# Performance work log

Measured on AMD Instinct MI355X. Metric: run time of the kernel, lower is better.

Reference implementation:

```python
import jax, jax.numpy as jnp
import numpy as np

TEMP = 0.1
EPS = 1e-12


def setup_inputs() -> dict:
    key = jax.random.key(0)
    k0, k1 = jax.random.split(key)
    instances_view0 = jax.random.normal(k0, (128, 32, 512), dtype=jnp.float32)
    instances_view1 = jax.random.normal(k1, (128, 32, 512), dtype=jnp.float32)
    return {"instances_view0": instances_view0, "instances_view1": instances_view1}


def reference(instances_view0, instances_view1):
    B, I, D = instances_view0.shape
    n_per_view = B * I  # n_instances_per_view
    f0 = instances_view0.reshape(n_per_view, D)
    f1 = instances_view1.reshape(n_per_view, D)
    inst = jnp.concatenate((f0, f1), axis=0)  # [N, D], N = 2*B*I
    # L2 normalize rows (torch F.normalize with eps clamp)
    norm = jnp.maximum(jnp.linalg.norm(inst, axis=1, keepdims=True), EPS)
    z = inst / norm
    sim_exp = jnp.exp(z @ z.T / TEMP)  # [N, N]
    denom = sim_exp.sum(axis=1) - jnp.diagonal(sim_exp)  # exclude self-similarity
    # positives: pairs offset by n_per_view in both directions
    idx = jnp.arange(n_per_view)
    upper = sim_exp[idx, idx + n_per_view]   # diagonal(offset=+n)
    lower = sim_exp[idx + n_per_view, idx]   # diagonal(offset=-n)
    nom = jnp.concatenate((upper, lower), axis=0)  # [N]
    loss = -jnp.log(nom / denom)
    return loss.mean()  # reduction='batchmean'
```

## Files before the change

kernel.cpp:

```cpp
#include <hip/hip_runtime.h>
#include <hip/hip_bf16.h>
#include <cstdint>

#define NROWS 8192
#define NPER  4096
#define DIM   512
#define TEMP_INV 10.0f
#define FP8_SCALE 16.0f
#define DOT_UNSCALE (1.0f / 256.0f)
#define NB    64
#define NBLK  2080
#define PAIR_OFF 32

typedef float f32x4 __attribute__((ext_vector_type(4)));

__global__ __launch_bounds__(256) void k_normalize(const float* __restrict__ v0,
                                                   const float* __restrict__ v1,
                                                   unsigned char* __restrict__ z,
                                                   float* __restrict__ rowsum,
                                                   float* __restrict__ out) {
  if (blockIdx.x < 32) rowsum[blockIdx.x * 256 + threadIdx.x] = 0.f;
  if (blockIdx.x == 0 && threadIdx.x == 0) out[0] = 0.f;
  const int wid  = (blockIdx.x * 256 + threadIdx.x) >> 6;
  const int lane = threadIdx.x & 63;
  if (wid >= NROWS) return;
  const float* src = (wid < NPER) ? (v0 + (size_t)wid * DIM)
                                  : (v1 + (size_t)(wid - NPER) * DIM);
  float4 a = *(const float4*)(src + lane * 8);
  float4 b = *(const float4*)(src + lane * 8 + 4);
  float ss = a.x*a.x + a.y*a.y + a.z*a.z + a.w*a.w
           + b.x*b.x + b.y*b.y + b.z*b.z + b.w*b.w;
  #pragma unroll
  for (int m = 1; m < 64; m <<= 1) ss += __shfl_xor(ss, m);
  float inv = FP8_SCALE / fmaxf(sqrtf(ss), 1e-12f);
  int w0 = __builtin_amdgcn_cvt_pk_fp8_f32(a.x * inv, a.y * inv, 0, false);
  w0     = __builtin_amdgcn_cvt_pk_fp8_f32(a.z * inv, a.w * inv, w0, true);
  int w1 = __builtin_amdgcn_cvt_pk_fp8_f32(b.x * inv, b.y * inv, 0, false);
  w1     = __builtin_amdgcn_cvt_pk_fp8_f32(b.z * inv, b.w * inv, w1, true);
  uint2 p; p.x = (unsigned)w0; p.y = (unsigned)w1;
  *(uint2*)(z + (size_t)wid * DIM + lane * 8) = p;
}

__global__ __launch_bounds__(256, 3) void k_gemm_sym(const unsigned char* __restrict__ z,
                                                     float* __restrict__ rowsum,
                                                     float* __restrict__ s) {
  __shared__ __align__(16) unsigned char As[128 * 128];
  __shared__ __align__(16) unsigned char Bs[128 * 128];

  const int tid  = threadIdx.x;
  const int lane = tid & 63;
  const int w    = tid >> 6;
  const int wr   = w >> 1;
  const int wc   = w & 1;

  const int orig = blockIdx.x;
  const int t = (orig & 7) * (NBLK / 8) + (orig >> 3);

  int a = 0;
  while (a < 7 && 484 * (a + 1) - 32 * (a + 1) * a <= t) ++a;
  int l = t - (484 * a - 32 * a * (a - 1));
  int ri, rj, sj;
  if (l < 36) {
    sj = a;
    ri = 0;
    while (l >= 8 - ri) { l -= 8 - ri; ++ri; }
    rj = ri + l;
  } else {
    l -= 36;
    sj = a + 1 + (l >> 6);
    const int ll = l & 63;
    ri = ll >> 3; rj = ll & 7;
  }
  const int bi = a * 8 + ri;
  const int bj = sj * 8 + rj;
  const int brow = bi * 128;
  const int bcol = bj * 128;
  const bool diag = (bi == bj);
  const bool pair = (bj - bi == PAIR_OFF);

  f32x4 acc[4][4];
  const f32x4 zero = {0.f, 0.f, 0.f, 0.f};
  #pragma unroll
  for (int m = 0; m < 4; ++m)
    #pragma unroll
    for (int n = 0; n < 4; ++n) acc[m][n] = zero;

  const int srow = (lane >> 3);
  const int skof = 16 * ((lane & 7) ^ srow);
  auto stage = [&](int k0) {
    #pragma unroll
    for (int i = 0; i < 4; ++i) {
      const int c = w * 4 + i;
      const int row_in = c * 8 + srow;
      const unsigned char* ga = z + (size_t)(brow + row_in) * DIM + k0 + skof;
      const unsigned char* gb = z + (size_t)(bcol + row_in) * DIM + k0 + skof;
      __builtin_amdgcn_global_load_lds(
          (const __attribute__((address_space(1))) void*)ga,
          (__attribute__((address_space(3))) void*)(&As[c * 1024]), 16, 0, 0);
      __builtin_amdgcn_global_load_lds(
          (const __attribute__((address_space(1))) void*)gb,
          (__attribute__((address_space(3))) void*)(&Bs[c * 1024]), 16, 0, 0);
    }
  };

  const int r0 = lane & 15;
  const int g  = lane >> 4;
  int colk[4];
  #pragma unroll
  for (int kk = 0; kk < 4; ++kk)
    colk[kk] = (((kk * 2 + (g >> 1)) ^ (r0 & 7)) << 4) + ((g & 1) << 3);

  for (int kt = 0; kt < 4; ++kt) {
    stage(kt * 128);
    asm volatile("s_waitcnt vmcnt(0)" ::: "memory");
    __builtin_amdgcn_s_barrier();

    const char* Ab = (const char*)&As[0] + (size_t)(wr * 64 + r0) * 128;
    const char* Bb = (const char*)&Bs[0] + (size_t)(wc * 64 + r0) * 128;
    #pragma unroll
    for (int kk = 0; kk < 4; ++kk) {
      const int cb = colk[kk];
      long bfrag[4];
      #pragma unroll
      for (int n = 0; n < 4; ++n)
        bfrag[n] = *(const long*)(Bb + n * (16 * 128) + cb);
      #pragma unroll
      for (int m = 0; m < 4; ++m) {
        long afrag = *(const long*)(Ab + m * (16 * 128) + cb);
        #pragma unroll
        for (int n = 0; n < 4; ++n)
          acc[m][n] = __builtin_amdgcn_mfma_f32_16x16x32_fp8_fp8(
              afrag, bfrag[n], acc[m][n], 0, 0, 0);
      }
    }
    asm volatile("s_waitcnt lgkmcnt(0)" ::: "memory");
    __builtin_amdgcn_sched_barrier(0);
    __builtin_amdgcn_s_barrier();
  }

  float (*racc)[128] = (float (*)[128])As;
  float (*cacc)[128] = ((float (*)[128])As) + 2;

  float cs[4] = {0.f, 0.f, 0.f, 0.f};
  const int grow0 = brow + wr * 64;
  const int gcol0 = bcol + wc * 64;
  const float expc = TEMP_INV * DOT_UNSCALE;
  #pragma unroll
  for (int m = 0; m < 4; ++m) {
    #pragma unroll
    for (int j = 0; j < 4; ++j) {
      const int grow = grow0 + m * 16 + g * 4 + j;
      float v = 0.f;
      #pragma unroll
      for (int n = 0; n < 4; ++n) {
        const int gcol = gcol0 + n * 16 + r0;
        const float rawacc = acc[m][n][j];
        const float e = __expf(rawacc * expc);
        if (grow != gcol) { v += e; cs[n] += e; }
        if (pair && (grow + NPER == gcol)) {
          const float raw = rawacc * DOT_UNSCALE;
          s[grow] = raw;
          s[gcol] = raw;
        }
      }
      v += __shfl_xor(v, 1);
      v += __shfl_xor(v, 2);
      v += __shfl_xor(v, 4);
      v += __shfl_xor(v, 8);
      if (r0 == 0) racc[wc][wr * 64 + m * 16 + g * 4 + j] = v;
    }
  }
  #pragma unroll
  for (int n = 0; n < 4; ++n) {
    float v = cs[n];
    v += __shfl_xor(v, 16);
    v += __shfl_xor(v, 32);
    if (lane < 16) cacc[wr][wc * 64 + n * 16 + lane] = v;
  }
  __syncthreads();
  if (tid < 128) {
    atomicAdd(&rowsum[brow + tid], racc[0][tid] + racc[1][tid]);
  } else if (!diag) {
    const int i = tid - 128;
    atomicAdd(&rowsum[bcol + i], cacc[0][i] + cacc[1][i]);
  }
}

__global__ __launch_bounds__(256) void k_loss(const float* __restrict__ rowsum,
                                              const float* __restrict__ s,
                                              float* __restrict__ out) {
  __shared__ float red[4];
  const int i = blockIdx.x * 256 + threadIdx.x;
  float v = logf(rowsum[i]) - s[i] * TEMP_INV;
  #pragma unroll
  for (int m = 1; m < 64; m <<= 1) v += __shfl_xor(v, m);
  const int w = threadIdx.x >> 6;
  if ((threadIdx.x & 63) == 0) red[w] = v;
  __syncthreads();
  if (threadIdx.x == 0)
    atomicAdd(out, (red[0] + red[1] + red[2] + red[3]) * (1.0f / (float)NROWS));
}

extern "C" void kernel_launch(void* const* d_in, const int* in_sizes, int n_in,
                              void* d_out, int out_size, void* d_ws, size_t ws_size,
                              hipStream_t stream) {
  const float* v0 = (const float*)d_in[0];
  const float* v1 = (const float*)d_in[1];
  float* out = (float*)d_out;

  unsigned char* z = (unsigned char*)d_ws;
  float* rowsum = (float*)((char*)d_ws + (size_t)NROWS * DIM);
  float* s      = rowsum + NROWS;

  k_normalize<<<NROWS / 4, 256, 0, stream>>>(v0, v1, z, rowsum, out);
  k_gemm_sym<<<NBLK, 256, 0, stream>>>(z, rowsum, s);
  k_loss<<<NROWS / 256, 256, 0, stream>>>(rowsum, s, out);
}
```

Baseline: 51.14 us.

## Triple-buffer K slabs in symmetric FP8 GEMM to overlap loads with MFMA

Splits the K loop into eight 64-wide slabs held in a three-stage LDS ring and prefetches two slabs ahead with direct global-to-LDS loads. A partial vmcnt wait lets compute on the current slab overlap the outstanding loads, and the trailing barrier per iteration is removed. LDS use drops from 32KB to 48KB-equivalent layout changes (3x16KB), which may affect occupancy, and the swizzle is adjusted for 64-byte rows. The epilogue reuses As, now a 2D array, as scratch space.

```diff
diff --git a/kernel.cpp b/kernel.cpp
--- a/kernel.cpp
+++ b/kernel.cpp
@@ -44,8 +44,8 @@
 __global__ __launch_bounds__(256, 3) void k_gemm_sym(const unsigned char* __restrict__ z,
                                                      float* __restrict__ rowsum,
                                                      float* __restrict__ s) {
-  __shared__ __align__(16) unsigned char As[128 * 128];
-  __shared__ __align__(16) unsigned char Bs[128 * 128];
+  __shared__ __align__(16) unsigned char As[3][128 * 64];
+  __shared__ __align__(16) unsigned char Bs[3][128 * 64];
 
   const int tid  = threadIdx.x;
   const int lane = tid & 63;
@@ -85,48 +85,54 @@
     #pragma unroll
     for (int n = 0; n < 4; ++n) acc[m][n] = zero;
 
-  const int srow = (lane >> 3);
-  const int skof = 16 * ((lane & 7) ^ srow);
-  auto stage = [&](int k0) {
-    #pragma unroll
-    for (int i = 0; i < 4; ++i) {
-      const int c = w * 4 + i;
-      const int row_in = c * 8 + srow;
-      const unsigned char* ga = z + (size_t)(brow + row_in) * DIM + k0 + skof;
-      const unsigned char* gb = z + (size_t)(bcol + row_in) * DIM + k0 + skof;
+  const int srow3 = lane >> 2;
+  const int skof3 = 16 * ((lane & 3) ^ (srow3 & 3));
+  auto stage = [&](int slab, int kt) {
+    const int k0 = kt * 64;
+    #pragma unroll
+    for (int i = 0; i < 2; ++i) {
+      const int R0 = (w * 2 + i) * 16;
+      const int row_in = R0 + srow3;
+      const unsigned char* ga = z + (size_t)(brow + row_in) * DIM + k0 + skof3;
+      const unsigned char* gb = z + (size_t)(bcol + row_in) * DIM + k0 + skof3;
       __builtin_amdgcn_global_load_lds(
           (const __attribute__((address_space(1))) void*)ga,
-          (__attribute__((address_space(3))) void*)(&As[c * 1024]), 16, 0, 0);
+          (__attribute__((address_space(3))) void*)(&As[slab][R0 * 64]), 16, 0, 0);
       __builtin_amdgcn_global_load_lds(
           (const __attribute__((address_space(1))) void*)gb,
-          (__attribute__((address_space(3))) void*)(&Bs[c * 1024]), 16, 0, 0);
+          (__attribute__((address_space(3))) void*)(&Bs[slab][R0 * 64]), 16, 0, 0);
     }
   };
 
+  stage(0, 0);
+  stage(1, 1);
+
   const int r0 = lane & 15;
   const int g  = lane >> 4;
-  int colk[4];
-  #pragma unroll
-  for (int kk = 0; kk < 4; ++kk)
-    colk[kk] = (((kk * 2 + (g >> 1)) ^ (r0 & 7)) << 4) + ((g & 1) << 3);
-
-  for (int kt = 0; kt < 4; ++kt) {
-    stage(kt * 128);
-    asm volatile("s_waitcnt vmcnt(0)" ::: "memory");
+  int cb[2];
+  #pragma unroll
+  for (int kk = 0; kk < 2; ++kk)
+    cb[kk] = (((kk * 2 + (g >> 1)) ^ (r0 & 3)) << 4) + ((g & 1) * 8);
+
+  for (int kt = 0; kt < 8; ++kt) {
+    const int cur = kt % 3;
+    if (kt < 7) asm volatile("s_waitcnt vmcnt(4)" ::: "memory");
+    else        asm volatile("s_waitcnt vmcnt(0)" ::: "memory");
     __builtin_amdgcn_s_barrier();
-
-    const char* Ab = (const char*)&As[0] + (size_t)(wr * 64 + r0) * 128;
-    const char* Bb = (const char*)&Bs[0] + (size_t)(wc * 64 + r0) * 128;
-    #pragma unroll
-    for (int kk = 0; kk < 4; ++kk) {
-      const int cb = colk[kk];
+    __builtin_amdgcn_sched_barrier(0);
+    if (kt < 6) stage((kt + 2) % 3, kt + 2);
+
+    const char* Ab = (const char*)&As[cur][0] + (size_t)(wr * 64 + r0) * 64;
+    const char* Bb = (const char*)&Bs[cur][0] + (size_t)(wc * 64 + r0) * 64;
+    #pragma unroll
+    for (int kk = 0; kk < 2; ++kk) {
       long bfrag[4];
       #pragma unroll
       for (int n = 0; n < 4; ++n)
-        bfrag[n] = *(const long*)(Bb + n * (16 * 128) + cb);
+        bfrag[n] = *(const long*)(Bb + n * 1024 + cb[kk]);
       #pragma unroll
       for (int m = 0; m < 4; ++m) {
-        long afrag = *(const long*)(Ab + m * (16 * 128) + cb);
+        long afrag = *(const long*)(Ab + m * 1024 + cb[kk]);
         #pragma unroll
         for (int n = 0; n < 4; ++n)
           acc[m][n] = __builtin_amdgcn_mfma_f32_16x16x32_fp8_fp8(
@@ -135,7 +141,6 @@
     }
     asm volatile("s_waitcnt lgkmcnt(0)" ::: "memory");
     __builtin_amdgcn_sched_barrier(0);
-    __builtin_amdgcn_s_barrier();
   }
 
   float (*racc)[128] = (float (*)[128])As;
```

After: 63.35 us. 1.24x slower.
